# Optimization experiments

Measured on AMD Instinct MI355X. Metric: run time of the kernel, lower is better.

The kernel has to match this reference:

```python
import jax, jax.numpy as jnp
import numpy as np

B, S, H2 = 32, 8192, 256  # batch, max_enc_steps, 2*hidden_dim
INIT_STD = 1e-4           # trunc_norm_init_std


def setup_inputs() -> dict:
    key = jax.random.key(0)
    k1, k2, k3 = jax.random.split(key, 3)
    h_d_t = jax.random.normal(k1, (B, H2), dtype=jnp.float32)
    h_enc = jax.random.normal(k2, (B, S, H2), dtype=jnp.float32)
    enc_padding_mask = jnp.ones((B, S), dtype=jnp.float32)
    sum_exp_att = jnp.ones((B, S), dtype=jnp.float32)
    # Bilinear weight (attn_dim=1 squeezed): (2H, 2H), trunc-normal init
    W = jax.random.normal(k3, (H2, H2), dtype=jnp.float32) * INIT_STD
    return {"h_d_t": h_d_t, "h_enc": h_enc, "enc_padding_mask": enc_padding_mask,
            "sum_exp_att": sum_exp_att, "W": W}


def reference(h_d_t, h_enc, enc_padding_mask, sum_exp_att, W):
    # Batched bilinear scores: score[b,s] = h_d_t[b] @ W @ h_enc[b,s]
    # replaces the per-timestep nn.Bilinear loop with one fused contraction.
    scores = jnp.einsum('bd,de,bse->bs', h_d_t, W, h_enc)  # (B, S)
    exp_att = jnp.exp(scores)
    # intra-temporal normalization by accumulated past exp attention
    att = exp_att / sum_exp_att
    new_sum_exp_att = sum_exp_att + exp_att
    # mask pads and renormalize
    alphat_e = att * enc_padding_mask
    alphat_e = alphat_e / jnp.sum(alphat_e, axis=1, keepdims=True)
    # context vector: weighted sum over encoder states
    ct_e = jnp.einsum('bs,bsd->bd', alphat_e, h_enc)  # (B, 2H)
    return ct_e, alphat_e, new_sum_exp_att
```

## Files before the change

### kernel.cpp

```cpp
#include <hip/hip_runtime.h>

#define B_ 32
#define S_ 8192
#define H_ 256

#define SPB 128
#define NBLK (S_ / SPB)

typedef float f4v __attribute__((ext_vector_type(4)));

__device__ __forceinline__ float4 ntld(const float4* p) {
    f4v v = __builtin_nontemporal_load(reinterpret_cast<const f4v*>(p));
    return make_float4(v.x, v.y, v.z, v.w);
}

__device__ __forceinline__ float row16_allsum(float x) {
    float t;
    t = __int_as_float(__builtin_amdgcn_update_dpp(0, __float_as_int(x), 0x121, 0xF, 0xF, false)); x += t;
    t = __int_as_float(__builtin_amdgcn_update_dpp(0, __float_as_int(x), 0x122, 0xF, 0xF, false)); x += t;
    t = __int_as_float(__builtin_amdgcn_update_dpp(0, __float_as_int(x), 0x124, 0xF, 0xF, false)); x += t;
    t = __int_as_float(__builtin_amdgcn_update_dpp(0, __float_as_int(x), 0x128, 0xF, 0xF, false)); x += t;
    return x;
}

__global__ __launch_bounds__(256) void gemv_hdtW(
    const float* __restrict__ hdt,
    const float* __restrict__ W,
    float* __restrict__ v_part)
{
    const int b  = blockIdx.x;
    const int ec = blockIdx.y;
    const int d  = threadIdx.x;

    __shared__ float lh[32];
    if (d < 32) lh[d] = hdt[b * H_ + ec * 32 + d];
    __syncthreads();

    float acc = 0.f;
    const float* Wp = W + (size_t)(ec * 32) * H_ + d;
#pragma unroll
    for (int e = 0; e < 32; ++e) acc = fmaf(lh[e], Wp[(size_t)e * H_], acc);

    v_part[(size_t)(ec * B_ + b) * H_ + d] = acc;
}

__global__ __launch_bounds__(256) void attn_main(
    const float* __restrict__ v_part,
    const float* __restrict__ h_enc,
    const float* __restrict__ sum_exp,
    const float* __restrict__ mask,
    float* __restrict__ out_alphat,
    float* __restrict__ out_newsum,
    float* __restrict__ part_den,
    float* __restrict__ part_ct)
{
    const int b    = blockIdx.y;
    const int bx   = blockIdx.x;
    const int tid  = threadIdx.x;
    const int lane = tid & 63;
    const int wave = tid >> 6;
    const int sub  = lane & 15;
    const int grp  = lane >> 4;
    const int pid  = wave * 4 + grp;
    const int s0   = bx * SPB;

    __shared__ float lmult[SPB];
    __shared__ float lse[SPB];
    __shared__ float lalpha[SPB];
    __shared__ float lnew[SPB];
    __shared__ __align__(16) float lct[16][H_];
    __shared__ float lden[16];

    if (tid < SPB) {
        const float se = sum_exp[(size_t)b * S_ + s0 + tid];
        const float mk = mask[(size_t)b * S_ + s0 + tid];
        lse[tid]   = se;
        lmult[tid] = mk / se;
    }
    __syncthreads();

    const float4* vp4 = reinterpret_cast<const float4*>(v_part);
    float4 vf0 = {0,0,0,0}, vf1 = {0,0,0,0}, vf2 = {0,0,0,0}, vf3 = {0,0,0,0};
#pragma unroll
    for (int ec = 0; ec < 8; ++ec) {
        const int base = (ec * B_ + b) * (H_ / 4);
        float4 p;
        p = vp4[base + 0*16 + sub]; vf0.x += p.x; vf0.y += p.y; vf0.z += p.z; vf0.w += p.w;
        p = vp4[base + 1*16 + sub]; vf1.x += p.x; vf1.y += p.y; vf1.z += p.z; vf1.w += p.w;
        p = vp4[base + 2*16 + sub]; vf2.x += p.x; vf2.y += p.y; vf2.z += p.z; vf2.w += p.w;
        p = vp4[base + 3*16 + sub]; vf3.x += p.x; vf3.y += p.y; vf3.z += p.z; vf3.w += p.w;
    }

    const float* __restrict__ hb = h_enc + (size_t)b * S_ * H_;
    const float4* pa = reinterpret_cast<const float4*>(hb + (size_t)s0 * H_)
                       + (size_t)(pid * 2) * 64;

    float4 ct0 = {0,0,0,0}, ct1 = {0,0,0,0}, ct2 = {0,0,0,0}, ct3 = {0,0,0,0};
    float  den = 0.f;

    float4 a0 = ntld(pa + 0*16 + sub), a1 = ntld(pa + 1*16 + sub);
    float4 a2 = ntld(pa + 2*16 + sub), a3 = ntld(pa + 3*16 + sub);
    float4 b0 = ntld(pa + 64 + 0*16 + sub), b1 = ntld(pa + 64 + 1*16 + sub);
    float4 b2 = ntld(pa + 64 + 2*16 + sub), b3 = ntld(pa + 64 + 3*16 + sub);

#pragma unroll
    for (int i = 0; i < SPB / 32; ++i) {
        float4 na0, na1, na2, na3, nb0, nb1, nb2, nb3;
        if (i < SPB / 32 - 1) {
            const float4* qa = pa + (size_t)(i + 1) * 32 * 64;
            na0 = ntld(qa + 0*16 + sub); na1 = ntld(qa + 1*16 + sub);
            na2 = ntld(qa + 2*16 + sub); na3 = ntld(qa + 3*16 + sub);
            nb0 = ntld(qa + 64 + 0*16 + sub); nb1 = ntld(qa + 64 + 1*16 + sub);
            nb2 = ntld(qa + 64 + 2*16 + sub); nb3 = ntld(qa + 64 + 3*16 + sub);
        }

        const int ra = i * 32 + pid * 2;
        const int rb = ra + 1;

        float da, db;
        da = fmaf(vf0.x, a0.x, fmaf(vf0.y, a0.y, fmaf(vf0.z, a0.z, vf0.w * a0.w)));
        da = fmaf(vf1.x, a1.x, fmaf(vf1.y, a1.y, fmaf(vf1.z, a1.z, fmaf(vf1.w, a1.w, da))));
        da = fmaf(vf2.x, a2.x, fmaf(vf2.y, a2.y, fmaf(vf2.z, a2.z, fmaf(vf2.w, a2.w, da))));
        da = fmaf(vf3.x, a3.x, fmaf(vf3.y, a3.y, fmaf(vf3.z, a3.z, fmaf(vf3.w, a3.w, da))));
        db = fmaf(vf0.x, b0.x, fmaf(vf0.y, b0.y, fmaf(vf0.z, b0.z, vf0.w * b0.w)));
        db = fmaf(vf1.x, b1.x, fmaf(vf1.y, b1.y, fmaf(vf1.z, b1.z, fmaf(vf1.w, b1.w, db))));
        db = fmaf(vf2.x, b2.x, fmaf(vf2.y, b2.y, fmaf(vf2.z, b2.z, fmaf(vf2.w, b2.w, db))));
        db = fmaf(vf3.x, b3.x, fmaf(vf3.y, b3.y, fmaf(vf3.z, b3.z, fmaf(vf3.w, b3.w, db))));

        da = row16_allsum(da);
        db = row16_allsum(db);

        const float ea = __expf(da);
        const float eb = __expf(db);
        const float atta = ea * lmult[ra];
        const float attb = eb * lmult[rb];
        if (sub == 0) {
            lalpha[ra] = atta;  lnew[ra] = lse[ra] + ea;
            lalpha[rb] = attb;  lnew[rb] = lse[rb] + eb;
        }
        den += atta + attb;
        ct0.x = fmaf(atta, a0.x, fmaf(attb, b0.x, ct0.x));
        ct0.y = fmaf(atta, a0.y, fmaf(attb, b0.y, ct0.y));
        ct0.z = fmaf(atta, a0.z, fmaf(attb, b0.z, ct0.z));
        ct0.w = fmaf(atta, a0.w, fmaf(attb, b0.w, ct0.w));
        ct1.x = fmaf(atta, a1.x, fmaf(attb, b1.x, ct1.x));
        ct1.y = fmaf(atta, a1.y, fmaf(attb, b1.y, ct1.y));
        ct1.z = fmaf(atta, a1.z, fmaf(attb, b1.z, ct1.z));
        ct1.w = fmaf(atta, a1.w, fmaf(attb, b1.w, ct1.w));
        ct2.x = fmaf(atta, a2.x, fmaf(attb, b2.x, ct2.x));
        ct2.y = fmaf(atta, a2.y, fmaf(attb, b2.y, ct2.y));
        ct2.z = fmaf(atta, a2.z, fmaf(attb, b2.z, ct2.z));
        ct2.w = fmaf(atta, a2.w, fmaf(attb, b2.w, ct2.w));
        ct3.x = fmaf(atta, a3.x, fmaf(attb, b3.x, ct3.x));
        ct3.y = fmaf(atta, a3.y, fmaf(attb, b3.y, ct3.y));
        ct3.z = fmaf(atta, a3.z, fmaf(attb, b3.z, ct3.z));
        ct3.w = fmaf(atta, a3.w, fmaf(attb, b3.w, ct3.w));

        if (i < SPB / 32 - 1) {
            a0 = na0; a1 = na1; a2 = na2; a3 = na3;
            b0 = nb0; b1 = nb1; b2 = nb2; b3 = nb3;
        }
    }

    float4* dst = reinterpret_cast<float4*>(&lct[pid][0]);
    dst[0*16 + sub] = ct0;
    dst[1*16 + sub] = ct1;
    dst[2*16 + sub] = ct2;
    dst[3*16 + sub] = ct3;
    if (sub == 0) lden[pid] = den;
    __syncthreads();

    float tot = 0.f;
#pragma unroll
    for (int p = 0; p < 16; ++p) tot += lct[p][tid];
    part_ct[((size_t)b * NBLK + bx) * H_ + tid] = tot;

    if (tid == 0) {
        float d = 0.f;
#pragma unroll
        for (int p = 0; p < 16; ++p) d += lden[p];
        part_den[b * NBLK + bx] = d;
    }

    if (tid < SPB) {
        out_alphat[(size_t)b * S_ + s0 + tid] = lalpha[tid];
        out_newsum[(size_t)b * S_ + s0 + tid] = lnew[tid];
    }
}

__global__ __launch_bounds__(256) void finalize(
    const float* __restrict__ part_den,
    const float* __restrict__ part_ct,
    float* __restrict__ out_ct,
    float* __restrict__ out_alphat)
{
    const int b   = blockIdx.x;
    const int sec = blockIdx.y;
    const int tid = threadIdx.x;

    __shared__ float pd[NBLK];
    if (tid < NBLK) pd[tid] = part_den[b * NBLK + tid];
    __syncthreads();

    float den = 0.f;
#pragma unroll
    for (int k = 0; k < NBLK; ++k) den += pd[k];
    const float inv = 1.f / den;

    if (sec == 16) {
        float ct = 0.f;
        const float* pc = part_ct + (size_t)b * NBLK * H_ + tid;
#pragma unroll 8
        for (int k = 0; k < NBLK; ++k) ct += pc[(size_t)k * H_];
        out_ct[b * H_ + tid] = ct * inv;
    } else {
        float* oa = out_alphat + (size_t)b * S_ + sec * 512;
        oa[tid]       *= inv;
        oa[tid + 256] *= inv;
    }
}

extern "C" void kernel_launch(void* const* d_in, const int* in_sizes, int n_in,
                              void* d_out, int out_size, void* d_ws, size_t ws_size,
                              hipStream_t stream) {
    const float* h_d_t   = (const float*)d_in[0];
    const float* h_enc   = (const float*)d_in[1];
    const float* mask    = (const float*)d_in[2];
    const float* sum_exp = (const float*)d_in[3];
    const float* W       = (const float*)d_in[4];

    float* out        = (float*)d_out;
    float* out_ct     = out;
    float* out_alphat = out + B_ * H_;
    float* out_newsum = out + B_ * H_ + B_ * S_;

    float* ws       = (float*)d_ws;
    float* v_part   = ws;
    float* part_den = v_part + 8 * B_ * H_;
    float* part_ct  = part_den + B_ * NBLK;

    gemv_hdtW<<<dim3(B_, 8), 256, 0, stream>>>(h_d_t, W, v_part);
    attn_main<<<dim3(NBLK, B_), 256, 0, stream>>>(v_part, h_enc, sum_exp, mask,
                                                  out_alphat, out_newsum,
                                                  part_den, part_ct);
    finalize<<<dim3(B_, 17), 256, 0, stream>>>(part_den, part_ct, out_ct, out_alphat);
}
```

Baseline: 349.0 us.

## Stream h_enc tiles into LDS with async global_load_lds double buffering

Replaces the register-prefetched nontemporal float4 loads of encoder rows with asynchronous global-to-LDS copies into a two-slot shared-memory tile of 16 rows. Each step waits on vmcnt, synchronises with a barrier, reads the row from LDS, then computes the score, exp and context accumulation. The aim is to overlap the h_enc stream with compute while freeing registers. It adds 32 KB of LDS, two barriers per tile and an extra LDS read pass, and only 64 KB of loads are in flight per block, which may reduce memory-level parallelism.

```diff
diff --git a/kernel.cpp b/kernel.cpp
--- a/kernel.cpp
+++ b/kernel.cpp
@@ -1,17 +1,23 @@
 #include <hip/hip_runtime.h>
+#include <stdint.h>
 
 #define B_ 32
 #define S_ 8192
 #define H_ 256
 
-#define SPB 128
-#define NBLK (S_ / SPB)
-
-typedef float f4v __attribute__((ext_vector_type(4)));
-
-__device__ __forceinline__ float4 ntld(const float4* p) {
-    f4v v = __builtin_nontemporal_load(reinterpret_cast<const f4v*>(p));
-    return make_float4(v.x, v.y, v.z, v.w);
+#define SPB   128
+#define NBLK  (S_ / SPB)
+#define TROWS 16
+#define NT    (SPB / TROWS)
+
+#define BARRIER()     asm volatile("s_barrier" ::: "memory")
+#define WAIT_VM(n)    asm volatile("s_waitcnt vmcnt(" #n ")" ::: "memory")
+
+__device__ __forceinline__ void async_row16(const float* gptr, float* lptr) {
+    __builtin_amdgcn_global_load_lds(
+        (const __attribute__((address_space(1))) void*)gptr,
+        (__attribute__((address_space(3))) void*)lptr,
+        16, 0, 0);
 }
 
 __device__ __forceinline__ float row16_allsum(float x) {
@@ -64,11 +70,12 @@
     const int pid  = wave * 4 + grp;
     const int s0   = bx * SPB;
 
+    __shared__ __align__(16) float tile[2][TROWS * H_];
+    __shared__ __align__(16) float lct[16][H_];
     __shared__ float lmult[SPB];
     __shared__ float lse[SPB];
     __shared__ float lalpha[SPB];
     __shared__ float lnew[SPB];
-    __shared__ __align__(16) float lct[16][H_];
     __shared__ float lden[16];
 
     if (tid < SPB) {
@@ -77,7 +84,6 @@
         lse[tid]   = se;
         lmult[tid] = mk / se;
     }
-    __syncthreads();
 
     const float4* vp4 = reinterpret_cast<const float4*>(v_part);
     float4 vf0 = {0,0,0,0}, vf1 = {0,0,0,0}, vf2 = {0,0,0,0}, vf3 = {0,0,0,0};
@@ -90,76 +96,64 @@
         p = vp4[base + 2*16 + sub]; vf2.x += p.x; vf2.y += p.y; vf2.z += p.z; vf2.w += p.w;
         p = vp4[base + 3*16 + sub]; vf3.x += p.x; vf3.y += p.y; vf3.z += p.z; vf3.w += p.w;
     }
-
-    const float* __restrict__ hb = h_enc + (size_t)b * S_ * H_;
-    const float4* pa = reinterpret_cast<const float4*>(hb + (size_t)s0 * H_)
-                       + (size_t)(pid * 2) * 64;
+    __syncthreads();
+
+    const float* __restrict__ hb = h_enc + (size_t)(b * S_ + s0) * H_;
+
+#pragma unroll
+    for (int k = 0; k < 4; ++k) {
+        const int r = wave * 4 + k;
+        async_row16(hb + (size_t)r * H_ + lane * 4, &tile[0][r * H_]);
+    }
 
     float4 ct0 = {0,0,0,0}, ct1 = {0,0,0,0}, ct2 = {0,0,0,0}, ct3 = {0,0,0,0};
     float  den = 0.f;
 
-    float4 a0 = ntld(pa + 0*16 + sub), a1 = ntld(pa + 1*16 + sub);
-    float4 a2 = ntld(pa + 2*16 + sub), a3 = ntld(pa + 3*16 + sub);
-    float4 b0 = ntld(pa + 64 + 0*16 + sub), b1 = ntld(pa + 64 + 1*16 + sub);
-    float4 b2 = ntld(pa + 64 + 2*16 + sub), b3 = ntld(pa + 64 + 3*16 + sub);
-
-#pragma unroll
-    for (int i = 0; i < SPB / 32; ++i) {
-        float4 na0, na1, na2, na3, nb0, nb1, nb2, nb3;
-        if (i < SPB / 32 - 1) {
-            const float4* qa = pa + (size_t)(i + 1) * 32 * 64;
-            na0 = ntld(qa + 0*16 + sub); na1 = ntld(qa + 1*16 + sub);
-            na2 = ntld(qa + 2*16 + sub); na3 = ntld(qa + 3*16 + sub);
-            nb0 = ntld(qa + 64 + 0*16 + sub); nb1 = ntld(qa + 64 + 1*16 + sub);
-            nb2 = ntld(qa + 64 + 2*16 + sub); nb3 = ntld(qa + 64 + 3*16 + sub);
+#pragma unroll
+    for (int t = 0; t < NT; ++t) {
+        if (t < NT - 1) {
+            const int tb = (t + 1) & 1;
+#pragma unroll
+            for (int k = 0; k < 4; ++k) {
+                const int r = wave * 4 + k;
+                async_row16(hb + (size_t)((t + 1) * TROWS + r) * H_ + lane * 4,
+                            &tile[tb][r * H_]);
+            }
+            WAIT_VM(4);
+        } else {
+            WAIT_VM(0);
         }
-
-        const int ra = i * 32 + pid * 2;
-        const int rb = ra + 1;
-
-        float da, db;
-        da = fmaf(vf0.x, a0.x, fmaf(vf0.y, a0.y, fmaf(vf0.z, a0.z, vf0.w * a0.w)));
-        da = fmaf(vf1.x, a1.x, fmaf(vf1.y, a1.y, fmaf(vf1.z, a1.z, fmaf(vf1.w, a1.w, da))));
-        da = fmaf(vf2.x, a2.x, fmaf(vf2.y, a2.y, fmaf(vf2.z, a2.z, fmaf(vf2.w, a2.w, da))));
-        da = fmaf(vf3.x, a3.x, fmaf(vf3.y, a3.y, fmaf(vf3.z, a3.z, fmaf(vf3.w, a3.w, da))));
-        db = fmaf(vf0.x, b0.x, fmaf(vf0.y, b0.y, fmaf(vf0.z, b0.z, vf0.w * b0.w)));
-        db = fmaf(vf1.x, b1.x, fmaf(vf1.y, b1.y, fmaf(vf1.z, b1.z, fmaf(vf1.w, b1.w, db))));
-        db = fmaf(vf2.x, b2.x, fmaf(vf2.y, b2.y, fmaf(vf2.z, b2.z, fmaf(vf2.w, b2.w, db))));
-        db = fmaf(vf3.x, b3.x, fmaf(vf3.y, b3.y, fmaf(vf3.z, b3.z, fmaf(vf3.w, b3.w, db))));
-
-        da = row16_allsum(da);
-        db = row16_allsum(db);
-
-        const float ea = __expf(da);
-        const float eb = __expf(db);
-        const float atta = ea * lmult[ra];
-        const float attb = eb * lmult[rb];
+        BARRIER();
+
+        const int ra = t * TROWS + pid;
+        const float4* R = reinterpret_cast<const float4*>(&tile[t & 1][pid * H_]);
+        const float4 a0 = R[0*16 + sub], a1 = R[1*16 + sub];
+        const float4 a2 = R[2*16 + sub], a3 = R[3*16 + sub];
+
+        float dot;
+        dot = fmaf(vf0.x, a0.x, fmaf(vf0.y, a0.y, fmaf(vf0.z, a0.z, vf0.w * a0.w)));
+        dot = fmaf(vf1.x, a1.x, fmaf(vf1.y, a1.y, fmaf(vf1.z, a1.z, fmaf(vf1.w, a1.w, dot))));
+        dot = fmaf(vf2.x, a2.x, fmaf(vf2.y, a2.y, fmaf(vf2.z, a2.z, fmaf(vf2.w, a2.w, dot))));
+        dot = fmaf(vf3.x, a3.x, fmaf(vf3.y, a3.y, fmaf(vf3.z, a3.z, fmaf(vf3.w, a3.w, dot))));
+        dot = row16_allsum(dot);
+
+        const float e   = __expf(dot);
+        const float att = e * lmult[ra];
         if (sub == 0) {
-            lalpha[ra] = atta;  lnew[ra] = lse[ra] + ea;
-            lalpha[rb] = attb;  lnew[rb] = lse[rb] + eb;
+            lalpha[ra] = att;
+            lnew[ra]   = lse[ra] + e;
         }
-        den += atta + attb;
-        ct0.x = fmaf(atta, a0.x, fmaf(attb, b0.x, ct0.x));
-        ct0.y = fmaf(atta, a0.y, fmaf(attb, b0.y, ct0.y));
-        ct0.z = fmaf(atta, a0.z, fmaf(attb, b0.z, ct0.z));
-        ct0.w = fmaf(atta, a0.w, fmaf(attb, b0.w, ct0.w));
-        ct1.x = fmaf(atta, a1.x, fmaf(attb, b1.x, ct1.x));
-        ct1.y = fmaf(atta, a1.y, fmaf(attb, b1.y, ct1.y));
-        ct1.z = fmaf(atta, a1.z, fmaf(attb, b1.z, ct1.z));
-        ct1.w = fmaf(atta, a1.w, fmaf(attb, b1.w, ct1.w));
-        ct2.x = fmaf(atta, a2.x, fmaf(attb, b2.x, ct2.x));
-        ct2.y = fmaf(atta, a2.y, fmaf(attb, b2.y, ct2.y));
-        ct2.z = fmaf(atta, a2.z, fmaf(attb, b2.z, ct2.z));
-        ct2.w = fmaf(atta, a2.w, fmaf(attb, b2.w, ct2.w));
-        ct3.x = fmaf(atta, a3.x, fmaf(attb, b3.x, ct3.x));
-        ct3.y = fmaf(atta, a3.y, fmaf(attb, b3.y, ct3.y));
-        ct3.z = fmaf(atta, a3.z, fmaf(attb, b3.z, ct3.z));
-        ct3.w = fmaf(atta, a3.w, fmaf(attb, b3.w, ct3.w));
-
-        if (i < SPB / 32 - 1) {
-            a0 = na0; a1 = na1; a2 = na2; a3 = na3;
-            b0 = nb0; b1 = nb1; b2 = nb2; b3 = nb3;
-        }
+        den += att;
+        ct0.x = fmaf(att, a0.x, ct0.x); ct0.y = fmaf(att, a0.y, ct0.y);
+        ct0.z = fmaf(att, a0.z, ct0.z); ct0.w = fmaf(att, a0.w, ct0.w);
+        ct1.x = fmaf(att, a1.x, ct1.x); ct1.y = fmaf(att, a1.y, ct1.y);
+        ct1.z = fmaf(att, a1.z, ct1.z); ct1.w = fmaf(att, a1.w, ct1.w);
+        ct2.x = fmaf(att, a2.x, ct2.x); ct2.y = fmaf(att, a2.y, ct2.y);
+        ct2.z = fmaf(att, a2.z, ct2.z); ct2.w = fmaf(att, a2.w, ct2.w);
+        ct3.x = fmaf(att, a3.x, ct3.x); ct3.y = fmaf(att, a3.y, ct3.y);
+        ct3.z = fmaf(att, a3.z, ct3.z); ct3.w = fmaf(att, a3.w, ct3.w);
+
+        BARRIER();
     }
 
     float4* dst = reinterpret_cast<float4*>(&lct[pid][0]);
```

Result: slower. 376.0 us (+7.7%).
